# Performance work log

Hardware: AMD Instinct MI355X
Metric: run time of the kernel (lower is better)

## Reference

```python
import jax, jax.numpy as jnp
import numpy as np

MARGIN = 60000.0


def setup_inputs() -> dict:
    key = jax.random.key(0)
    x = jax.random.normal(key, (4, 4096, 256), dtype=jnp.float32)
    return {"x": x}


def reference(x):
    # x: [batch, seq_len, feat]
    # Original: for a>b, d(a,b) = sum over (batch, feat) of (x[:,a]-x[:,b])^2,
    # label = 0 if a-b==1 else 1,
    # loss += label*d + (1-label)*max(0, margin-d); normalized by S*(S-1)*1000.
    S = x.shape[1]
    # Pairwise squared distances via Gram trick, summed over batch and feat:
    # D[a,b] = s[a] + s[b] - 2*G[a,b], s[t] = sum_{n,f} x[n,t,f]^2
    s = jnp.sum(x * x, axis=(0, 2))                      # [S]
    G = jnp.einsum('nsf,ntf->st', x, x)                  # [S, S]
    D = s[:, None] + s[None, :] - 2.0 * G                # [S, S]

    idx = jnp.arange(S)
    lower = idx[:, None] > idx[None, :]                  # a > b
    adjacent = (idx[:, None] - idx[None, :]) == 1        # a - b == 1 -> label 0
    label = jnp.where(adjacent, 0.0, 1.0)

    per_pair = label * D + (1.0 - label) * jnp.maximum(0.0, MARGIN - D)
    loss = jnp.sum(jnp.where(lower, per_pair, 0.0))
    denom = jnp.asarray(S * (S - 1) * 1000, dtype=x.dtype)
    return loss / denom
```

## Files before the change

### kernel.cpp

```cpp
#include <hip/hip_runtime.h>
#include <stdint.h>

#define SEQ   4096
#define MARG  60000.0f
#define DENOM 16773120000.0


__device__ __forceinline__ float dot4(float4 a) {
  return a.x * a.x + a.y * a.y + a.z * a.z + a.w * a.w;
}
__device__ __forceinline__ float dist2(float4 a, float4 b) {
  float dx = a.x - b.x, dy = a.y - b.y, dz = a.z - b.z, dw = a.w - b.w;
  return dx * dx + dy * dy + dz * dz + dw * dw;
}
__device__ __forceinline__ float wred(float v) {
  #pragma unroll
  for (int o = 32; o; o >>= 1) v += __shfl_down(v, o, 64);
  return v;
}
__device__ __forceinline__ double wredd(double v) {
  #pragma unroll
  for (int o = 32; o; o >>= 1) v += __shfl_down(v, o, 64);
  return v;
}

__global__ __launch_bounds__(256) void pass1_kernel(
    const float* __restrict__ x, float* __restrict__ dpart,
    float* __restrict__ tpart, float* __restrict__ spart) {
  const int b    = blockIdx.x;
  const int n    = b >> 8;
  const int c    = b & 255;
  const int tid  = threadIdx.x;
  const int w    = tid >> 6, lane = tid & 63;
  const int s0   = c * 16 + w * 4;
  const float* rowp = x + (((size_t)(n * SEQ + s0)) << 8) + (lane << 2);

  const float4 v0 = *(const float4*)(rowp);
  const float4 v1 = *(const float4*)(rowp + 256);
  const float4 v2 = *(const float4*)(rowp + 512);
  const float4 v3 = *(const float4*)(rowp + 768);
  float4 vp;
  if (s0 > 0) vp = *(const float4*)(rowp - 256);
  else        vp = v0;

  float4 tacc;
  tacc.x = v0.x + v1.x + v2.x + v3.x;
  tacc.y = v0.y + v1.y + v2.y + v3.y;
  tacc.z = v0.z + v1.z + v2.z + v3.z;
  tacc.w = v0.w + v1.w + v2.w + v3.w;
  const float s2 = dot4(v0) + dot4(v1) + dot4(v2) + dot4(v3);

  const float r0 = wred(dist2(v0, vp));
  const float r1 = wred(dist2(v1, v0));
  const float r2 = wred(dist2(v2, v1));
  const float r3 = wred(dist2(v3, v2));
  if (lane == 0) {
    float* dp = dpart + n * SEQ + s0;
    if (s0 > 0) dp[0] = r0;
    dp[1] = r1; dp[2] = r2; dp[3] = r3;
  }
  const float s2r = wred(s2);

  __shared__ float4 tl[4][64];
  __shared__ float  sl[4];
  tl[w][lane] = tacc;
  if (lane == 0) sl[w] = s2r;
  __syncthreads();
  if (w == 0) {
    const float4 a = tl[0][lane], bq = tl[1][lane], cq = tl[2][lane], dq = tl[3][lane];
    float4 t;
    t.x = a.x + bq.x + cq.x + dq.x;
    t.y = a.y + bq.y + cq.y + dq.y;
    t.z = a.z + bq.z + cq.z + dq.z;
    t.w = a.w + bq.w + cq.w + dq.w;
    *(float4*)(tpart + b * 256 + (lane << 2)) = t;
    if (lane == 0) spart[b] = sl[0] + sl[1] + sl[2] + sl[3];
  }
}

__global__ __launch_bounds__(256) void treduce_kernel(
    const float* __restrict__ tpart, double* __restrict__ t2part) {
  const int B = blockIdx.x;
  const int n = B >> 2, fq = B & 3;
  const int tid  = threadIdx.x;
  const int part = tid >> 6, fl = tid & 63;
  const int f = fq * 64 + fl;
  float t = 0.f;
  const int c0 = part * 64;
  #pragma unroll 8
  for (int c = c0; c < c0 + 64; ++c) t += tpart[((n * 256 + c) << 8) + f];
  __shared__ float tl[4][64];
  tl[part][fl] = t;
  __syncthreads();
  if (part == 0) {
    const float tt = tl[0][fl] + tl[1][fl] + tl[2][fl] + tl[3][fl];
    double t2 = (double)tt * (double)tt;
    t2 = wredd(t2);
    if (fl == 0) t2part[B] = t2;
  }
}

__global__ __launch_bounds__(256) void finalize_kernel(
    const float* __restrict__ dpart, const float* __restrict__ spart,
    const double* __restrict__ t2part, float* __restrict__ out) {
  const int tid = threadIdx.x;
  double dsum = 0.0, hsum = 0.0, ss = 0.0;
  for (int a = 1 + tid; a < SEQ; a += 256) {
    const float D = dpart[a] + dpart[SEQ + a] + dpart[2 * SEQ + a] + dpart[3 * SEQ + a];
    dsum += (double)D;
    hsum += (double)fmaxf(0.f, MARG - D);
  }
  #pragma unroll
  for (int i = tid; i < 1024; i += 256) ss += (double)spart[i];
  dsum = wredd(dsum); hsum = wredd(hsum); ss = wredd(ss);
  __shared__ double rl[3][4];
  const int w = tid >> 6, lane = tid & 63;
  if (lane == 0) { rl[0][w] = dsum; rl[1][w] = hsum; rl[2][w] = ss; }
  __syncthreads();
  if (tid == 0) {
    const double D  = rl[0][0] + rl[0][1] + rl[0][2] + rl[0][3];
    const double H  = rl[1][0] + rl[1][1] + rl[1][2] + rl[1][3];
    const double S2 = rl[2][0] + rl[2][1] + rl[2][2] + rl[2][3];
    double t2 = 0.0;
    #pragma unroll
    for (int i = 0; i < 16; ++i) t2 += t2part[i];
    const double num = 4096.0 * S2 - t2 - D + H;
    out[0] = (float)(num / DENOM);
  }
}

extern "C" void kernel_launch(void* const* d_in, const int* in_sizes, int n_in,
                              void* d_out, int out_size, void* d_ws, size_t ws_size,
                              hipStream_t stream) {
  const float* x = (const float*)d_in[0];
  float* out = (float*)d_out;
  char* ws = (char*)d_ws;
  float*  dpart  = (float*)(ws);
  float*  spart  = (float*)(ws + 65536);
  double* t2part = (double*)(ws + 69632);
  float*  tpart  = (float*)(ws + 131072);

  pass1_kernel<<<1024, 256, 0, stream>>>(x, dpart, tpart, spart);
  treduce_kernel<<<16, 256, 0, stream>>>(tpart, t2part);
  finalize_kernel<<<1, 256, 0, stream>>>(dpart, spart, t2part, out);
}
```

Before: 74.87 us.

## Fuse three-kernel reduction into one kernel with atomics and last-block finalize

Merges the pass1, treduce and finalize kernels into a single launch. Per-feature column sums are accumulated with float atomics into a small global buffer instead of per-block partials, and the last block (found with an atomic counter and threadfences) computes the final loss. This removes two kernel launches and the round trip of the 1 MB partial buffer, at the cost of an added memset, atomic contention on 1024 addresses, and non-deterministic float summation order.

```diff
diff --git a/kernel.cpp b/kernel.cpp
--- a/kernel.cpp
+++ b/kernel.cpp
@@ -4,6 +4,7 @@
 #define SEQ   4096
 #define MARG  60000.0f
 #define DENOM 16773120000.0
+#define NBLK  1024
 
 
 __device__ __forceinline__ float dot4(float4 a) {
@@ -24,9 +25,10 @@
   return v;
 }
 
-__global__ __launch_bounds__(256) void pass1_kernel(
+__global__ __launch_bounds__(256) void fused_kernel(
     const float* __restrict__ x, float* __restrict__ dpart,
-    float* __restrict__ tpart, float* __restrict__ spart) {
+    float* __restrict__ spart, float* __restrict__ tglobal,
+    unsigned int* __restrict__ cnt, float* __restrict__ out) {
   const int b    = blockIdx.x;
   const int n    = b >> 8;
   const int c    = b & 255;
@@ -68,63 +70,44 @@
   __syncthreads();
   if (w == 0) {
     const float4 a = tl[0][lane], bq = tl[1][lane], cq = tl[2][lane], dq = tl[3][lane];
-    float4 t;
-    t.x = a.x + bq.x + cq.x + dq.x;
-    t.y = a.y + bq.y + cq.y + dq.y;
-    t.z = a.z + bq.z + cq.z + dq.z;
-    t.w = a.w + bq.w + cq.w + dq.w;
-    *(float4*)(tpart + b * 256 + (lane << 2)) = t;
+    float* tg = tglobal + n * 256 + (lane << 2);
+    unsafeAtomicAdd(tg + 0, a.x + bq.x + cq.x + dq.x);
+    unsafeAtomicAdd(tg + 1, a.y + bq.y + cq.y + dq.y);
+    unsafeAtomicAdd(tg + 2, a.z + bq.z + cq.z + dq.z);
+    unsafeAtomicAdd(tg + 3, a.w + bq.w + cq.w + dq.w);
     if (lane == 0) spart[b] = sl[0] + sl[1] + sl[2] + sl[3];
   }
-}
 
-__global__ __launch_bounds__(256) void treduce_kernel(
-    const float* __restrict__ tpart, double* __restrict__ t2part) {
-  const int B = blockIdx.x;
-  const int n = B >> 2, fq = B & 3;
-  const int tid  = threadIdx.x;
-  const int part = tid >> 6, fl = tid & 63;
-  const int f = fq * 64 + fl;
-  float t = 0.f;
-  const int c0 = part * 64;
-  #pragma unroll 8
-  for (int c = c0; c < c0 + 64; ++c) t += tpart[((n * 256 + c) << 8) + f];
-  __shared__ float tl[4][64];
-  tl[part][fl] = t;
+  __threadfence();
+  __shared__ unsigned int lastflag;
+  if (tid == 0) lastflag = atomicAdd(cnt, 1u);
   __syncthreads();
-  if (part == 0) {
-    const float tt = tl[0][fl] + tl[1][fl] + tl[2][fl] + tl[3][fl];
-    double t2 = (double)tt * (double)tt;
-    t2 = wredd(t2);
-    if (fl == 0) t2part[B] = t2;
+  if (lastflag != NBLK - 1) return;
+  __threadfence();
+
+  double t2 = 0.0, ss = 0.0, dsum = 0.0, hsum = 0.0;
+  #pragma unroll
+  for (int i = tid; i < 1024; i += 256) {
+    const float t = tglobal[i];
+    t2 += (double)t * (double)t;
+    ss += (double)spart[i];
   }
-}
-
-__global__ __launch_bounds__(256) void finalize_kernel(
-    const float* __restrict__ dpart, const float* __restrict__ spart,
-    const double* __restrict__ t2part, float* __restrict__ out) {
-  const int tid = threadIdx.x;
-  double dsum = 0.0, hsum = 0.0, ss = 0.0;
-  for (int a = 1 + tid; a < SEQ; a += 256) {
+  for (int a = tid; a < SEQ; a += 256) {
+    if (a == 0) continue;
     const float D = dpart[a] + dpart[SEQ + a] + dpart[2 * SEQ + a] + dpart[3 * SEQ + a];
     dsum += (double)D;
     hsum += (double)fmaxf(0.f, MARG - D);
   }
-  #pragma unroll
-  for (int i = tid; i < 1024; i += 256) ss += (double)spart[i];
-  dsum = wredd(dsum); hsum = wredd(hsum); ss = wredd(ss);
-  __shared__ double rl[3][4];
-  const int w = tid >> 6, lane = tid & 63;
-  if (lane == 0) { rl[0][w] = dsum; rl[1][w] = hsum; rl[2][w] = ss; }
+  t2 = wredd(t2); ss = wredd(ss); dsum = wredd(dsum); hsum = wredd(hsum);
+  __shared__ double rl[4][4];
+  if (lane == 0) { rl[0][w] = t2; rl[1][w] = ss; rl[2][w] = dsum; rl[3][w] = hsum; }
   __syncthreads();
   if (tid == 0) {
-    const double D  = rl[0][0] + rl[0][1] + rl[0][2] + rl[0][3];
-    const double H  = rl[1][0] + rl[1][1] + rl[1][2] + rl[1][3];
-    const double S2 = rl[2][0] + rl[2][1] + rl[2][2] + rl[2][3];
-    double t2 = 0.0;
-    #pragma unroll
-    for (int i = 0; i < 16; ++i) t2 += t2part[i];
-    const double num = 4096.0 * S2 - t2 - D + H;
+    const double T2 = rl[0][0] + rl[0][1] + rl[0][2] + rl[0][3];
+    const double S2 = rl[1][0] + rl[1][1] + rl[1][2] + rl[1][3];
+    const double DS = rl[2][0] + rl[2][1] + rl[2][2] + rl[2][3];
+    const double HS = rl[3][0] + rl[3][1] + rl[3][2] + rl[3][3];
+    const double num = 4096.0 * S2 - T2 - DS + HS;
     out[0] = (float)(num / DENOM);
   }
 }
@@ -135,12 +118,11 @@
   const float* x = (const float*)d_in[0];
   float* out = (float*)d_out;
   char* ws = (char*)d_ws;
-  float*  dpart  = (float*)(ws);
-  float*  spart  = (float*)(ws + 65536);
-  double* t2part = (double*)(ws + 69632);
-  float*  tpart  = (float*)(ws + 131072);
+  unsigned int* cnt  = (unsigned int*)ws;
+  float* tglobal     = (float*)(ws + 256);
+  float* spart       = (float*)(ws + 8192);
+  float* dpart       = (float*)(ws + 16384);
 
-  pass1_kernel<<<1024, 256, 0, stream>>>(x, dpart, tpart, spart);
-  treduce_kernel<<<16, 256, 0, stream>>>(tpart, t2part);
-  finalize_kernel<<<1, 256, 0, stream>>>(dpart, spart, t2part, out);
+  hipMemsetAsync(ws, 0, 256 + 4096, stream);
+  fused_kernel<<<NBLK, 256, 0, stream>>>(x, dpart, spart, tglobal, cnt, out);
 }
```

After: 165.0 us. +120.4%, slower.
